# Performance work log

Hardware: AMD Instinct MI355X
Metric: run time of the kernel (lower is better)

The kernel has to match this reference:

```python
import jax, jax.numpy as jnp
import numpy as np

B, S, D = 2, 2048, 2048
H, KVH = 16, 4
HD = D // H            # 128
N_REP = H // KVH       # 4


def apply_rope(x, cos, sin):
    # x: (b, s, h, hd); cos/sin: (1, s, 1, hd//2)
    b, s, h, hd = x.shape
    xr = x.reshape(b, s, h, hd // 2, 2)
    p1, p2 = xr[..., 0], xr[..., 1]
    # Original concatenates rotated halves (does NOT re-interleave).
    return jnp.concatenate([p1 * cos - p2 * sin, p2 * cos + p1 * sin], axis=-1)


def setup_inputs() -> dict:
    key = jax.random.key(0)
    ks = jax.random.split(key, 8)
    hidden_states = jax.random.normal(ks[0], (B, S, D), dtype=jnp.float32)
    # additive causal mask (0 on/below diagonal, -1e9 above)
    mask = jnp.where(jnp.tril(jnp.ones((S, S), dtype=bool)), 0.0, -1e9).astype(jnp.float32)
    attention_mask = mask[None, None, :, :]
    cos = jax.random.normal(ks[1], (1, S, 1, HD // 2), dtype=jnp.float32)
    sin = jax.random.normal(ks[2], (1, S, 1, HD // 2), dtype=jnp.float32)
    sc = 1.0 / np.sqrt(D)
    Wq = jax.random.normal(ks[3], (D, H * HD), dtype=jnp.float32) * sc
    Wk = jax.random.normal(ks[4], (D, KVH * HD), dtype=jnp.float32) * sc
    Wv = jax.random.normal(ks[5], (D, KVH * HD), dtype=jnp.float32) * sc
    Wo = jax.random.normal(ks[6], (H * HD, D), dtype=jnp.float32) * sc
    return {"hidden_states": hidden_states, "attention_mask": attention_mask,
            "cos": cos, "sin": sin, "Wq": Wq, "Wk": Wk, "Wv": Wv, "Wo": Wo}


def reference(hidden_states, attention_mask, cos, sin, Wq, Wk, Wv, Wo):
    b, s, _ = hidden_states.shape
    q = (hidden_states @ Wq).reshape(b, s, H, HD)
    k = (hidden_states @ Wk).reshape(b, s, KVH, HD)
    v = (hidden_states @ Wv).reshape(b, s, KVH, HD)
    q = apply_rope(q, cos, sin)
    k = apply_rope(k, cos, sin)
    # GQA: repeat kv heads contiguously (matches expand+reshape)
    k = jnp.repeat(k, N_REP, axis=2)
    v = jnp.repeat(v, N_REP, axis=2)
    # (b, h, s, hd)
    q = q.transpose(0, 2, 1, 3)
    k = k.transpose(0, 2, 1, 3)
    v = v.transpose(0, 2, 1, 3)
    scores = jnp.einsum('bhqd,bhkd->bhqk', q, k) / np.sqrt(HD).astype(np.float32)
    scores = scores + attention_mask
    attn = jax.nn.softmax(scores.astype(jnp.float32), axis=-1)
    out = jnp.einsum('bhqk,bhkd->bhqd', attn, v)
    out = out.transpose(0, 2, 1, 3).reshape(b, s, H * HD)
    return out @ Wo
```

## Files before the change

kernel.cpp:

```cpp
#include <hip/hip_runtime.h>
#include <cstddef>
#include <cstdint>

#define S_LEN 2048
#define DMODEL 2048
#define NH 16
#define NKV 4
#define HD 128
#define BATCH 2
#define MROWS (BATCH * S_LEN)
#define KVD (NKV * HD)
#define QKVSTR 3072
#define NQT (S_LEN / 64)

typedef __attribute__((ext_vector_type(8))) short bf16x8;
typedef __attribute__((ext_vector_type(4))) short shortx4;
typedef __attribute__((ext_vector_type(4))) float floatx4;
typedef __attribute__((ext_vector_type(8))) _Float16 half8;
typedef __attribute__((ext_vector_type(4))) _Float16 half4;
typedef __attribute__((ext_vector_type(2))) _Float16 half2v;

#define QSCALE 0.1275310255f

__device__ inline short f2bf(float f) {
  union { float f; unsigned u; } v; v.f = f;
  unsigned r = v.u + 0x7FFFu + ((v.u >> 16) & 1u);
  return (short)(r >> 16);
}

__device__ inline half2v pack2h(float lo, float hi) {
  union { decltype(__builtin_amdgcn_cvt_pkrtz(0.f, 0.f)) raw; half2v h; } u;
  u.raw = __builtin_amdgcn_cvt_pkrtz(lo, hi);
  return u.h;
}

__device__ __forceinline__ void glds16(const void* g, void* l) {
  __builtin_amdgcn_global_load_lds(
      reinterpret_cast<const int __attribute__((address_space(1)))*>(
          reinterpret_cast<uintptr_t>(g)),
      reinterpret_cast<int __attribute__((address_space(3)))*>(
          reinterpret_cast<uintptr_t>(l)),
      16, 0, 0);
}

__global__ __launch_bounds__(256) void cast_bf16(
    const float* __restrict__ x, short* __restrict__ y)
{
  const size_t i = ((size_t)blockIdx.x * 256 + threadIdx.x) * 8;
  const float4 a = *(const float4*)(x + i);
  const float4 b = *(const float4*)(x + i + 4);
  bf16x8 o;
  o[0] = f2bf(a.x); o[1] = f2bf(a.y); o[2] = f2bf(a.z); o[3] = f2bf(a.w);
  o[4] = f2bf(b.x); o[5] = f2bf(b.y); o[6] = f2bf(b.z); o[7] = f2bf(b.w);
  *(bf16x8*)(y + i) = o;
}

__global__ __launch_bounds__(256) void tcast(
    const float* __restrict__ W, short* __restrict__ Wt, int N)
{
  __shared__ float Ts[64][65];
  const int n0 = blockIdx.x * 64, k0 = blockIdx.y * 64;
  const int tid = threadIdx.x;
#pragma unroll
  for (int it = 0; it < 4; ++it) {
    const int r = it * 16 + (tid >> 4);
    *(float4*)&Ts[r][(tid & 15) * 4] =
        *(const float4*)&W[(size_t)(k0 + r) * N + n0 + (tid & 15) * 4];
  }
  __syncthreads();
  const int n = tid >> 2, kg = (tid & 3) * 16;
  bf16x8 o0, o1;
#pragma unroll
  for (int e = 0; e < 8; ++e) o0[e] = f2bf(Ts[kg + e][n]);
#pragma unroll
  for (int e = 0; e < 8; ++e) o1[e] = f2bf(Ts[kg + 8 + e][n]);
  short* dst = Wt + (size_t)(n0 + n) * DMODEL + k0 + kg;
  *(bf16x8*)dst = o0;
  *(bf16x8*)(dst + 8) = o1;
}

template <int BN, bool OUTF16>
__global__ __launch_bounds__(512, 2) void gemm_swz(
    const short* __restrict__ A, const short* __restrict__ Bt,
    void* __restrict__ Cv, int M, int N, int K)
{
  constexpr int NF = BN / 64;
  __shared__ short As[2][256 * 64];
  __shared__ short Bs[2][BN * 64];

  const int tid = threadIdx.x;
  const int lane = tid & 63;
  const int l16 = lane & 15, quad = lane >> 4;
  const int wave = tid >> 6;
  const int wmi = wave >> 2;
  const int wni = wave & 3;
  const int m0 = blockIdx.y * 256, n0 = blockIdx.x * BN;

  const int srow = tid >> 3;
  const int scol = ((tid & 7) ^ (srow & 7)) * 8;
  const int lofs = srow * 64 + (tid & 7) * 8;
  const short* Ab = A + (size_t)(m0 + srow) * K + scol;
  const short* Bb = Bt + (size_t)(n0 + srow) * K + scol;

  const int xs0 = ((0 * 4 + quad) ^ (l16 & 7)) * 8;
  const int xs1 = ((1 * 4 + quad) ^ (l16 & 7)) * 8;

  floatx4 acc[8][NF];
#pragma unroll
  for (int i = 0; i < 8; ++i)
#pragma unroll
    for (int j = 0; j < NF; ++j)
#pragma unroll
      for (int r = 0; r < 4; ++r) acc[i][j][r] = 0.f;

#pragma unroll
  for (int u = 0; u < 4; ++u)
    glds16(Ab + (size_t)(u * 64) * K, &As[0][u * 4096 + lofs]);
#pragma unroll
  for (int u = 0; u < NF; ++u)
    glds16(Bb + (size_t)(u * 64) * K, &Bs[0][u * 4096 + lofs]);
  __syncthreads();

  const int nkt = K >> 6;
  for (int kt = 0; kt < nkt; ++kt) {
    const int cur = kt & 1;
    const short* Asc = As[cur];
    const short* Bsc = Bs[cur];
    short* Asn = As[cur ^ 1];
    short* Bsn = Bs[cur ^ 1];
    const int knext = (kt + 1) << 6;
    const bool pre = (kt + 1 < nkt);

    bf16x8 bfr[NF][2];
#pragma unroll
    for (int n = 0; n < NF; ++n) {
      const int br = (wni * (NF * 16) + n * 16 + l16) * 64;
      bfr[n][0] = *(const bf16x8*)&Bsc[br + xs0];
      bfr[n][1] = *(const bf16x8*)&Bsc[br + xs1];
    }

#pragma unroll
    for (int p = 0; p < 4; ++p) {
      bf16x8 af[2][2];
#pragma unroll
      for (int i = 0; i < 2; ++i) {
        const int ar = (wmi * 128 + (p * 2 + i) * 16 + l16) * 64;
        af[i][0] = *(const bf16x8*)&Asc[ar + xs0];
        af[i][1] = *(const bf16x8*)&Asc[ar + xs1];
      }
      if (pre) {
        if (p == 0) {
          glds16(Ab + (size_t)(0 * 64) * K + knext, &Asn[0 * 4096 + lofs]);
          glds16(Ab + (size_t)(1 * 64) * K + knext, &Asn[1 * 4096 + lofs]);
        } else if (p == 1) {
          glds16(Ab + (size_t)(2 * 64) * K + knext, &Asn[2 * 4096 + lofs]);
          glds16(Ab + (size_t)(3 * 64) * K + knext, &Asn[3 * 4096 + lofs]);
        } else if (p == 2) {
          glds16(Bb + (size_t)(0 * 64) * K + knext, &Bsn[0 * 4096 + lofs]);
          if (NF == 3)
            glds16(Bb + (size_t)(1 * 64) * K + knext, &Bsn[1 * 4096 + lofs]);
        } else {
          glds16(Bb + (size_t)((NF - 1) * 64) * K + knext, &Bsn[(NF - 1) * 4096 + lofs]);
        }
      }
      __builtin_amdgcn_s_barrier();
      __builtin_amdgcn_s_setprio(1);
#pragma unroll
      for (int i = 0; i < 2; ++i)
#pragma unroll
        for (int n = 0; n < NF; ++n) {
          acc[p * 2 + i][n] = __builtin_amdgcn_mfma_f32_16x16x32_bf16(af[i][0], bfr[n][0], acc[p * 2 + i][n], 0, 0, 0);
          acc[p * 2 + i][n] = __builtin_amdgcn_mfma_f32_16x16x32_bf16(af[i][1], bfr[n][1], acc[p * 2 + i][n], 0, 0, 0);
        }
      __builtin_amdgcn_s_setprio(0);
      if (p < 3) __builtin_amdgcn_s_barrier();
    }
    __syncthreads();
  }

#pragma unroll
  for (int mi = 0; mi < 8; ++mi)
#pragma unroll
    for (int r = 0; r < 4; ++r) {
      const int row = m0 + wmi * 128 + mi * 16 + quad * 4 + r;
      if (OUTF16) {
        _Float16* cr = (_Float16*)Cv + (size_t)row * N + n0 + wni * (NF * 16) + l16;
#pragma unroll
        for (int ni = 0; ni < NF; ++ni) cr[ni * 16] = (_Float16)acc[mi][ni][r];
      } else {
        float* cr = (float*)Cv + (size_t)row * N + n0 + wni * (NF * 16) + l16;
#pragma unroll
        for (int ni = 0; ni < NF; ++ni) cr[ni * 16] = acc[mi][ni][r];
      }
    }
}

__global__ __launch_bounds__(256) void rope_k(
    _Float16* __restrict__ kh, const float* __restrict__ cosp,
    const float* __restrict__ sinp)
{
  const int row = blockIdx.x * 4 + (threadIdx.x >> 6);
  const int sl = row & (S_LEN - 1);
  const int t = threadIdx.x & 63;
  const int h = t >> 4, g = t & 15;
  _Float16* base = kh + (size_t)row * QKVSTR + h * HD;
  const half8 x = *(const half8*)(base + 8 * g);
  const float4 c4 = *(const float4*)&cosp[sl * 64 + 4 * g];
  const float4 s4 = *(const float4*)&sinp[sl * 64 + 4 * g];
  const float p1[4] = {(float)x[0], (float)x[2], (float)x[4], (float)x[6]};
  const float p2[4] = {(float)x[1], (float)x[3], (float)x[5], (float)x[7]};
  const float cc[4] = {c4.x, c4.y, c4.z, c4.w};
  const float ss[4] = {s4.x, s4.y, s4.z, s4.w};
  __syncthreads();
  half4 o1, o2;
#pragma unroll
  for (int u = 0; u < 4; ++u) {
    o1[u] = (_Float16)(p1[u] * cc[u] - p2[u] * ss[u]);
    o2[u] = (_Float16)(p2[u] * cc[u] + p1[u] * ss[u]);
  }
  *(half4*)(base + 4 * g) = o1;
  *(half4*)(base + 64 + 4 * g) = o2;
}

__global__ __launch_bounds__(256) void vtprep(
    const _Float16* __restrict__ v, _Float16* __restrict__ Vt)
{
  __shared__ _Float16 Ts[64][72];
  const int s0 = blockIdx.x * 64, c0 = blockIdx.y * 64;
  const int tid = threadIdx.x;
#pragma unroll
  for (int it = 0; it < 4; ++it) {
    const int r = it * 16 + (tid >> 4);
    *(half4*)&Ts[r][(tid & 15) * 4] =
        *(const half4*)&v[(size_t)(s0 + r) * QKVSTR + c0 + (tid & 15) * 4];
  }
  __syncthreads();
  const int dr = tid >> 2, sg = tid & 3;
  const int d = c0 + dr;
  const int kvh = d >> 7, dd = d & 127;
  const int bb = s0 >> 11, sl = s0 & (S_LEN - 1);
  half8 t0, t1;
#pragma unroll
  for (int kk = 0; kk < 8; ++kk) t0[kk] = Ts[sg * 16 + kk][dr];
#pragma unroll
  for (int kk = 0; kk < 8; ++kk) t1[kk] = Ts[sg * 16 + 8 + kk][dr];
  _Float16* dst = Vt + ((size_t)(bb * NKV + kvh) * HD + dd) * S_LEN + sl + sg * 16;
  *(half8*)dst = t0;
  *(half8*)(dst + 8) = t1;
}

__global__ __launch_bounds__(256, 3) void attn_mfma(
    const _Float16* __restrict__ Qh, const _Float16* __restrict__ Kr,
    const _Float16* __restrict__ Vt, const float* __restrict__ cosp,
    const float* __restrict__ sinp, short* __restrict__ aout)
{
  __shared__ _Float16 Ks[64][136];
  __shared__ _Float16 Vs[128][72];
  __shared__ _Float16 Ps[4][16][72];

  const int tid = threadIdx.x;
  const int wave = tid >> 6, lane = tid & 63;
  const int l16 = lane & 15, quad = lane >> 4;
  const int pair = blockIdx.x;
  const int h = blockIdx.y, b = blockIdx.z;
  const int kvh = h >> 2;

  const int skr = tid >> 2;
  const int skc = (tid & 3) * 32;
  const _Float16* kgp = Kr + (size_t)(b * S_LEN + skr) * QKVSTR + kvh * HD + skc;
  const int svr = tid >> 1;
  const int svc = (tid & 1) * 32;
  const _Float16* vgp = Vt + ((size_t)(b * NKV + kvh) * HD + svr) * S_LEN + svc;

  for (int pass = 0; pass < 2; ++pass) {
    const int qt = pass ? (NQT - 1 - pair) : pair;
    const int q0 = qt * 64 + wave * 16;
    const int srow = q0 + l16;

    half8 qf[4];
    {
      const _Float16* qraw = Qh + (size_t)(b * S_LEN + srow) * QKVSTR + h * HD;
      const int co = (srow & (S_LEN - 1)) * 64;
#pragma unroll
      for (int cc = 0; cc < 2; ++cc) {
        const half8 r0 = *(const half8*)(qraw + cc * 64 + quad * 16);
        const half8 r1 = *(const half8*)(qraw + cc * 64 + quad * 16 + 8);
        const float4 c0 = *(const float4*)&cosp[co + cc * 32 + quad * 8];
        const float4 c1 = *(const float4*)&cosp[co + cc * 32 + quad * 8 + 4];
        const float4 s0 = *(const float4*)&sinp[co + cc * 32 + quad * 8];
        const float4 s1 = *(const float4*)&sinp[co + cc * 32 + quad * 8 + 4];
        const float cA[8] = {c0.x, c0.y, c0.z, c0.w, c1.x, c1.y, c1.z, c1.w};
        const float sA[8] = {s0.x, s0.y, s0.z, s0.w, s1.x, s1.y, s1.z, s1.w};
#pragma unroll
        for (int j = 0; j < 8; ++j) {
          const float p1 = (float)((j < 4) ? r0[2 * j] : r1[2 * (j - 4)]);
          const float p2 = (float)((j < 4) ? r0[2 * j + 1] : r1[2 * (j - 4) + 1]);
          qf[cc][j]     = (_Float16)((p1 * cA[j] - p2 * sA[j]) * QSCALE);
          qf[cc + 2][j] = (_Float16)((p2 * cA[j] + p1 * sA[j]) * QSCALE);
        }
      }
    }

    floatx4 o[8];
#pragma unroll
    for (int d = 0; d < 8; ++d) o[d] = (floatx4){0.f, 0.f, 0.f, 0.f};
    float m_run = -3e38f, l_run = 0.f;

    for (int kt = 0; kt <= qt; ++kt) {
      const int k0 = kt * 64;
      __syncthreads();
      {
        const _Float16* g = kgp + (size_t)k0 * QKVSTR;
        _Float16* dst = &Ks[skr][skc];
#pragma unroll
        for (int u = 0; u < 4; ++u)
          *(half8*)(dst + u * 8) = *(const half8*)(g + u * 8);
      }
      {
        const _Float16* g = vgp + k0;
        _Float16* dst = &Vs[svr][svc];
#pragma unroll
        for (int u = 0; u < 4; ++u)
          *(half8*)(dst + u * 8) = *(const half8*)(g + u * 8);
      }
      __syncthreads();

      floatx4 s[4];
      __builtin_amdgcn_s_setprio(1);
#pragma unroll
      for (int i = 0; i < 4; ++i) {
        s[i] = (floatx4){0.f, 0.f, 0.f, 0.f};
#pragma unroll
        for (int c = 0; c < 4; ++c) {
          const half8 kf = *(const half8*)&Ks[i * 16 + l16][quad * 8 + c * 32];
          s[i] = __builtin_amdgcn_mfma_f32_16x16x32_f16(kf, qf[c], s[i], 0, 0, 0);
        }
      }
      __builtin_amdgcn_s_setprio(0);

      if (kt == qt) {
#pragma unroll
        for (int i = 0; i < 4; ++i) {
          const int kvbase = k0 + i * 16 + quad * 4;
#pragma unroll
          for (int r = 0; r < 4; ++r)
            if (kvbase + r > srow) s[i][r] = -3.0e38f;
        }
      }

      float m0 = fmaxf(fmaxf(s[0][0], s[0][1]), fmaxf(s[0][2], s[0][3]));
      float m1 = fmaxf(fmaxf(s[1][0], s[1][1]), fmaxf(s[1][2], s[1][3]));
      float m2 = fmaxf(fmaxf(s[2][0], s[2][1]), fmaxf(s[2][2], s[2][3]));
      float m3 = fmaxf(fmaxf(s[3][0], s[3][1]), fmaxf(s[3][2], s[3][3]));
      float rm = fmaxf(fmaxf(m0, m1), fmaxf(m2, m3));
      rm = fmaxf(rm, __shfl_xor(rm, 16));
      rm = fmaxf(rm, __shfl_xor(rm, 32));
      if (rm > m_run) {
        const float alpha = exp2f(m_run - rm);
        m_run = rm;
        l_run *= alpha;
#pragma unroll
        for (int d = 0; d < 8; ++d)
#pragma unroll
          for (int r = 0; r < 4; ++r) o[d][r] *= alpha;
      }
      float p[4][4];
      float rs = 0.f;
#pragma unroll
      for (int i = 0; i < 4; ++i)
#pragma unroll
        for (int r = 0; r < 4; ++r) {
          p[i][r] = exp2f(s[i][r] - m_run);
          rs += p[i][r];
        }
      rs += __shfl_xor(rs, 16);
      rs += __shfl_xor(rs, 32);
      l_run += rs;

#pragma unroll
      for (int i = 0; i < 4; ++i) {
        *(half2v*)&Ps[wave][l16][i * 16 + quad * 4]     = pack2h(p[i][0], p[i][1]);
        *(half2v*)&Ps[wave][l16][i * 16 + quad * 4 + 2] = pack2h(p[i][2], p[i][3]);
      }
      const half8 pf0 = *(const half8*)&Ps[wave][l16][quad * 8];
      const half8 pf1 = *(const half8*)&Ps[wave][l16][32 + quad * 8];

      __builtin_amdgcn_s_setprio(1);
#pragma unroll
      for (int d = 0; d < 8; ++d) {
        const half8 vf0 = *(const half8*)&Vs[d * 16 + l16][quad * 8];
        const half8 vf1 = *(const half8*)&Vs[d * 16 + l16][32 + quad * 8];
        o[d] = __builtin_amdgcn_mfma_f32_16x16x32_f16(vf0, pf0, o[d], 0, 0, 0);
        o[d] = __builtin_amdgcn_mfma_f32_16x16x32_f16(vf1, pf1, o[d], 0, 0, 0);
      }
      __builtin_amdgcn_s_setprio(0);
    }

    const float inv = 1.0f / l_run;
    short* orow = aout + (size_t)(b * S_LEN + srow) * DMODEL + h * HD;
#pragma unroll
    for (int d = 0; d < 8; ++d) {
      shortx4 pk;
      pk[0] = f2bf(o[d][0] * inv);
      pk[1] = f2bf(o[d][1] * inv);
      pk[2] = f2bf(o[d][2] * inv);
      pk[3] = f2bf(o[d][3] * inv);
      *(shortx4*)(orow + d * 16 + quad * 4) = pk;
    }
  }
}

extern "C" void kernel_launch(void* const* d_in, const int* in_sizes, int n_in,
                              void* d_out, int out_size, void* d_ws, size_t ws_size,
                              hipStream_t stream) {
  const float* hs   = (const float*)d_in[0];
  const float* cosp = (const float*)d_in[2];
  const float* sinp = (const float*)d_in[3];
  const float* Wq   = (const float*)d_in[4];
  const float* Wk   = (const float*)d_in[5];
  const float* Wv   = (const float*)d_in[6];
  const float* Wo   = (const float*)d_in[7];
  float* out = (float*)d_out;

  char* w = (char*)d_ws;
  short*    hsb = (short*)w;
  short*    Wt  = (short*)(w + 16777216);
  _Float16* qkv = (_Float16*)(w + 29360128);
  _Float16* Vt  = (_Float16*)(w + 54525952);
  short*    ao  = hsb;

  _Float16* qh = qkv;
  _Float16* kh = qkv + 2048;
  _Float16* vh = qkv + 2560;

  dim3 blk(256);
  cast_bf16<<<MROWS * DMODEL / (8 * 256), blk, 0, stream>>>(hs, hsb);
  tcast<<<dim3(DMODEL / 64, DMODEL / 64), blk, 0, stream>>>(Wq, Wt, DMODEL);
  tcast<<<dim3(KVD / 64, DMODEL / 64), blk, 0, stream>>>(Wk, Wt + (size_t)2048 * DMODEL, KVD);
  tcast<<<dim3(KVD / 64, DMODEL / 64), blk, 0, stream>>>(Wv, Wt + (size_t)2560 * DMODEL, KVD);
  gemm_swz<192, true><<<dim3(QKVSTR / 192, MROWS / 256), dim3(512), 0, stream>>>(hsb, Wt, qkv, MROWS, QKVSTR, DMODEL);
  rope_k<<<MROWS / 4, blk, 0, stream>>>(kh, cosp, sinp);
  vtprep<<<dim3(MROWS / 64, KVD / 64), blk, 0, stream>>>(vh, Vt);
  attn_mfma<<<dim3(NQT / 2, NH, BATCH), blk, 0, stream>>>(qh, kh, Vt, cosp, sinp, ao);
  tcast<<<dim3(DMODEL / 64, DMODEL / 64), blk, 0, stream>>>(Wo, Wt, DMODEL);
  gemm_swz<128, false><<<dim3(DMODEL / 128, MROWS / 256), dim3(512), 0, stream>>>(ao, Wt, out, MROWS, DMODEL, DMODEL);
}
```

Before: 327.7 us.

## Process 32 query rows per wave to reuse K/V tiles in attention

Each attention block now handles a 128-row query tile: every wave owns 32 rows, held as two 16-row MFMA fragments that share each K and V fragment loaded from LDS. This replaces the earlier two-pass pairing of light and heavy 64-row tiles with one block per tile on a flattened 512-block grid, where the order of query tiles is reversed for the second batch to spread the causal work. The intent is to halve K/V global and LDS traffic per query row and raise the ratio of MFMA work to loads. In exchange, register pressure doubles, so the occupancy hint drops from 3 to 2 blocks per SM, and per-block work is less even.

```diff
diff --git a/kernel.cpp b/kernel.cpp
--- a/kernel.cpp
+++ b/kernel.cpp
@@ -11,7 +11,6 @@
 #define MROWS (BATCH * S_LEN)
 #define KVD (NKV * HD)
 #define QKVSTR 3072
-#define NQT (S_LEN / 64)
 
 typedef __attribute__((ext_vector_type(8))) short bf16x8;
 typedef __attribute__((ext_vector_type(4))) short shortx4;
@@ -249,20 +248,22 @@
   *(half8*)(dst + 8) = t1;
 }
 
-__global__ __launch_bounds__(256, 3) void attn_mfma(
+__global__ __launch_bounds__(256, 2) void attn_mfma(
     const _Float16* __restrict__ Qh, const _Float16* __restrict__ Kr,
     const _Float16* __restrict__ Vt, const float* __restrict__ cosp,
     const float* __restrict__ sinp, short* __restrict__ aout)
 {
   __shared__ _Float16 Ks[64][136];
   __shared__ _Float16 Vs[128][72];
-  __shared__ _Float16 Ps[4][16][72];
+  __shared__ _Float16 Ps[4][32][72];
 
   const int tid = threadIdx.x;
   const int wave = tid >> 6, lane = tid & 63;
   const int l16 = lane & 15, quad = lane >> 4;
-  const int pair = blockIdx.x;
-  const int h = blockIdx.y, b = blockIdx.z;
+  const int kb = blockIdx.x;
+  const int b = kb >> 8;
+  const int h = (kb >> 4) & 15;
+  const int qt = b ? (15 - (kb & 15)) : (kb & 15);
   const int kvh = h >> 2;
 
   const int skr = tid >> 2;
@@ -272,139 +273,159 @@
   const int svc = (tid & 1) * 32;
   const _Float16* vgp = Vt + ((size_t)(b * NKV + kvh) * HD + svr) * S_LEN + svc;
 
-  for (int pass = 0; pass < 2; ++pass) {
-    const int qt = pass ? (NQT - 1 - pair) : pair;
-    const int q0 = qt * 64 + wave * 16;
-    const int srow = q0 + l16;
-
-    half8 qf[4];
+  const int qbase = qt * 128 + wave * 32;
+
+  half8 qf[2][4];
+#pragma unroll
+  for (int r16 = 0; r16 < 2; ++r16) {
+    const int srow = qbase + r16 * 16 + l16;
+    const _Float16* qraw = Qh + (size_t)(b * S_LEN + srow) * QKVSTR + h * HD;
+    const int co = srow * 64;
+#pragma unroll
+    for (int cc = 0; cc < 2; ++cc) {
+      const half8 r0 = *(const half8*)(qraw + cc * 64 + quad * 16);
+      const half8 r1 = *(const half8*)(qraw + cc * 64 + quad * 16 + 8);
+      const float4 c0 = *(const float4*)&cosp[co + cc * 32 + quad * 8];
+      const float4 c1 = *(const float4*)&cosp[co + cc * 32 + quad * 8 + 4];
+      const float4 s0 = *(const float4*)&sinp[co + cc * 32 + quad * 8];
+      const float4 s1 = *(const float4*)&sinp[co + cc * 32 + quad * 8 + 4];
+      const float cA[8] = {c0.x, c0.y, c0.z, c0.w, c1.x, c1.y, c1.z, c1.w};
+      const float sA[8] = {s0.x, s0.y, s0.z, s0.w, s1.x, s1.y, s1.z, s1.w};
+#pragma unroll
+      for (int j = 0; j < 8; ++j) {
+        const float p1 = (float)((j < 4) ? r0[2 * j] : r1[2 * (j - 4)]);
+        const float p2 = (float)((j < 4) ? r0[2 * j + 1] : r1[2 * (j - 4) + 1]);
+        qf[r16][cc][j]     = (_Float16)((p1 * cA[j] - p2 * sA[j]) * QSCALE);
+        qf[r16][cc + 2][j] = (_Float16)((p2 * cA[j] + p1 * sA[j]) * QSCALE);
+      }
+    }
+  }
+
+  floatx4 o[2][8];
+#pragma unroll
+  for (int r16 = 0; r16 < 2; ++r16)
+#pragma unroll
+    for (int d = 0; d < 8; ++d) o[r16][d] = (floatx4){0.f, 0.f, 0.f, 0.f};
+  float m_run[2] = {-3e38f, -3e38f};
+  float l_run[2] = {0.f, 0.f};
+
+  const int ktmax = 2 * qt + 1;
+  for (int kt = 0; kt <= ktmax; ++kt) {
+    const int k0 = kt * 64;
+    __syncthreads();
     {
-      const _Float16* qraw = Qh + (size_t)(b * S_LEN + srow) * QKVSTR + h * HD;
-      const int co = (srow & (S_LEN - 1)) * 64;
-#pragma unroll
-      for (int cc = 0; cc < 2; ++cc) {
-        const half8 r0 = *(const half8*)(qraw + cc * 64 + quad * 16);
-        const half8 r1 = *(const half8*)(qraw + cc * 64 + quad * 16 + 8);
-        const float4 c0 = *(const float4*)&cosp[co + cc * 32 + quad * 8];
-        const float4 c1 = *(const float4*)&cosp[co + cc * 32 + quad * 8 + 4];
-        const float4 s0 = *(const float4*)&sinp[co + cc * 32 + quad * 8];
-        const float4 s1 = *(const float4*)&sinp[co + cc * 32 + quad * 8 + 4];
-        const float cA[8] = {c0.x, c0.y, c0.z, c0.w, c1.x, c1.y, c1.z, c1.w};
-        const float sA[8] = {s0.x, s0.y, s0.z, s0.w, s1.x, s1.y, s1.z, s1.w};
-#pragma unroll
-        for (int j = 0; j < 8; ++j) {
-          const float p1 = (float)((j < 4) ? r0[2 * j] : r1[2 * (j - 4)]);
-          const float p2 = (float)((j < 4) ? r0[2 * j + 1] : r1[2 * (j - 4) + 1]);
-          qf[cc][j]     = (_Float16)((p1 * cA[j] - p2 * sA[j]) * QSCALE);
-          qf[cc + 2][j] = (_Float16)((p2 * cA[j] + p1 * sA[j]) * QSCALE);
-        }
-      }
-    }
-
-    floatx4 o[8];
-#pragma unroll
-    for (int d = 0; d < 8; ++d) o[d] = (floatx4){0.f, 0.f, 0.f, 0.f};
-    float m_run = -3e38f, l_run = 0.f;
-
-    for (int kt = 0; kt <= qt; ++kt) {
-      const int k0 = kt * 64;
-      __syncthreads();
-      {
-        const _Float16* g = kgp + (size_t)k0 * QKVSTR;
-        _Float16* dst = &Ks[skr][skc];
-#pragma unroll
-        for (int u = 0; u < 4; ++u)
-          *(half8*)(dst + u * 8) = *(const half8*)(g + u * 8);
-      }
-      {
-        const _Float16* g = vgp + k0;
-        _Float16* dst = &Vs[svr][svc];
-#pragma unroll
-        for (int u = 0; u < 4; ++u)
-          *(half8*)(dst + u * 8) = *(const half8*)(g + u * 8);
-      }
-      __syncthreads();
-
-      floatx4 s[4];
-      __builtin_amdgcn_s_setprio(1);
-#pragma unroll
-      for (int i = 0; i < 4; ++i) {
-        s[i] = (floatx4){0.f, 0.f, 0.f, 0.f};
-#pragma unroll
-        for (int c = 0; c < 4; ++c) {
-          const half8 kf = *(const half8*)&Ks[i * 16 + l16][quad * 8 + c * 32];
-          s[i] = __builtin_amdgcn_mfma_f32_16x16x32_f16(kf, qf[c], s[i], 0, 0, 0);
-        }
-      }
-      __builtin_amdgcn_s_setprio(0);
-
-      if (kt == qt) {
+      const _Float16* g = kgp + (size_t)k0 * QKVSTR;
+      _Float16* dst = &Ks[skr][skc];
+#pragma unroll
+      for (int u = 0; u < 4; ++u)
+        *(half8*)(dst + u * 8) = *(const half8*)(g + u * 8);
+    }
+    {
+      const _Float16* g = vgp + k0;
+      _Float16* dst = &Vs[svr][svc];
+#pragma unroll
+      for (int u = 0; u < 4; ++u)
+        *(half8*)(dst + u * 8) = *(const half8*)(g + u * 8);
+    }
+    __syncthreads();
+
+    floatx4 s[2][4];
+    __builtin_amdgcn_s_setprio(1);
+#pragma unroll
+    for (int i = 0; i < 4; ++i) {
+      s[0][i] = (floatx4){0.f, 0.f, 0.f, 0.f};
+      s[1][i] = (floatx4){0.f, 0.f, 0.f, 0.f};
+#pragma unroll
+      for (int c = 0; c < 4; ++c) {
+        const half8 kf = *(const half8*)&Ks[i * 16 + l16][quad * 8 + c * 32];
+        s[0][i] = __builtin_amdgcn_mfma_f32_16x16x32_f16(kf, qf[0][c], s[0][i], 0, 0, 0);
+        s[1][i] = __builtin_amdgcn_mfma_f32_16x16x32_f16(kf, qf[1][c], s[1][i], 0, 0, 0);
+      }
+    }
+    __builtin_amdgcn_s_setprio(0);
+
+#pragma unroll
+    for (int r16 = 0; r16 < 2; ++r16) {
+      if (k0 + 63 > qbase + r16 * 16) {
+        const int srow = qbase + r16 * 16 + l16;
 #pragma unroll
         for (int i = 0; i < 4; ++i) {
           const int kvbase = k0 + i * 16 + quad * 4;
 #pragma unroll
           for (int r = 0; r < 4; ++r)
-            if (kvbase + r > srow) s[i][r] = -3.0e38f;
+            if (kvbase + r > srow) s[r16][i][r] = -3.0e38f;
         }
       }
-
-      float m0 = fmaxf(fmaxf(s[0][0], s[0][1]), fmaxf(s[0][2], s[0][3]));
-      float m1 = fmaxf(fmaxf(s[1][0], s[1][1]), fmaxf(s[1][2], s[1][3]));
-      float m2 = fmaxf(fmaxf(s[2][0], s[2][1]), fmaxf(s[2][2], s[2][3]));
-      float m3 = fmaxf(fmaxf(s[3][0], s[3][1]), fmaxf(s[3][2], s[3][3]));
+    }
+
+#pragma unroll
+    for (int r16 = 0; r16 < 2; ++r16) {
+      float m0 = fmaxf(fmaxf(s[r16][0][0], s[r16][0][1]), fmaxf(s[r16][0][2], s[r16][0][3]));
+      float m1 = fmaxf(fmaxf(s[r16][1][0], s[r16][1][1]), fmaxf(s[r16][1][2], s[r16][1][3]));
+      float m2 = fmaxf(fmaxf(s[r16][2][0], s[r16][2][1]), fmaxf(s[r16][2][2], s[r16][2][3]));
+      float m3 = fmaxf(fmaxf(s[r16][3][0], s[r16][3][1]), fmaxf(s[r16][3][2], s[r16][3][3]));
       float rm = fmaxf(fmaxf(m0, m1), fmaxf(m2, m3));
       rm = fmaxf(rm, __shfl_xor(rm, 16));
       rm = fmaxf(rm, __shfl_xor(rm, 32));
-      if (rm > m_run) {
-        const float alpha = exp2f(m_run - rm);
-        m_run = rm;
-        l_run *= alpha;
+      if (rm > m_run[r16]) {
+        const float alpha = exp2f(m_run[r16] - rm);
+        m_run[r16] = rm;
+        l_run[r16] *= alpha;
 #pragma unroll
         for (int d = 0; d < 8; ++d)
 #pragma unroll
-          for (int r = 0; r < 4; ++r) o[d][r] *= alpha;
-      }
-      float p[4][4];
+          for (int r = 0; r < 4; ++r) o[r16][d][r] *= alpha;
+      }
       float rs = 0.f;
 #pragma unroll
       for (int i = 0; i < 4; ++i)
 #pragma unroll
         for (int r = 0; r < 4; ++r) {
-          p[i][r] = exp2f(s[i][r] - m_run);
-          rs += p[i][r];
+          s[r16][i][r] = exp2f(s[r16][i][r] - m_run[r16]);
+          rs += s[r16][i][r];
         }
       rs += __shfl_xor(rs, 16);
       rs += __shfl_xor(rs, 32);
-      l_run += rs;
+      l_run[r16] += rs;
 
 #pragma unroll
       for (int i = 0; i < 4; ++i) {
-        *(half2v*)&Ps[wave][l16][i * 16 + quad * 4]     = pack2h(p[i][0], p[i][1]);
-        *(half2v*)&Ps[wave][l16][i * 16 + quad * 4 + 2] = pack2h(p[i][2], p[i][3]);
-      }
-      const half8 pf0 = *(const half8*)&Ps[wave][l16][quad * 8];
-      const half8 pf1 = *(const half8*)&Ps[wave][l16][32 + quad * 8];
-
-      __builtin_amdgcn_s_setprio(1);
-#pragma unroll
-      for (int d = 0; d < 8; ++d) {
-        const half8 vf0 = *(const half8*)&Vs[d * 16 + l16][quad * 8];
-        const half8 vf1 = *(const half8*)&Vs[d * 16 + l16][32 + quad * 8];
-        o[d] = __builtin_amdgcn_mfma_f32_16x16x32_f16(vf0, pf0, o[d], 0, 0, 0);
-        o[d] = __builtin_amdgcn_mfma_f32_16x16x32_f16(vf1, pf1, o[d], 0, 0, 0);
-      }
-      __builtin_amdgcn_s_setprio(0);
-    }
-
-    const float inv = 1.0f / l_run;
-    short* orow = aout + (size_t)(b * S_LEN + srow) * DMODEL + h * HD;
+        *(half2v*)&Ps[wave][r16 * 16 + l16][i * 16 + quad * 4] =
+            pack2h(s[r16][i][0], s[r16][i][1]);
+        *(half2v*)&Ps[wave][r16 * 16 + l16][i * 16 + quad * 4 + 2] =
+            pack2h(s[r16][i][2], s[r16][i][3]);
+      }
+    }
+
+    const half8 pf00 = *(const half8*)&Ps[wave][l16][quad * 8];
+    const half8 pf01 = *(const half8*)&Ps[wave][l16][32 + quad * 8];
+    const half8 pf10 = *(const half8*)&Ps[wave][16 + l16][quad * 8];
+    const half8 pf11 = *(const half8*)&Ps[wave][16 + l16][32 + quad * 8];
+
+    __builtin_amdgcn_s_setprio(1);
+#pragma unroll
+    for (int d = 0; d < 8; ++d) {
+      const half8 vf0 = *(const half8*)&Vs[d * 16 + l16][quad * 8];
+      const half8 vf1 = *(const half8*)&Vs[d * 16 + l16][32 + quad * 8];
+      o[0][d] = __builtin_amdgcn_mfma_f32_16x16x32_f16(vf0, pf00, o[0][d], 0, 0, 0);
+      o[0][d] = __builtin_amdgcn_mfma_f32_16x16x32_f16(vf1, pf01, o[0][d], 0, 0, 0);
+      o[1][d] = __builtin_amdgcn_mfma_f32_16x16x32_f16(vf0, pf10, o[1][d], 0, 0, 0);
+      o[1][d] = __builtin_amdgcn_mfma_f32_16x16x32_f16(vf1, pf11, o[1][d], 0, 0, 0);
+    }
+    __builtin_amdgcn_s_setprio(0);
+  }
+
+#pragma unroll
+  for (int r16 = 0; r16 < 2; ++r16) {
+    const float inv = 1.0f / l_run[r16];
+    short* orow = aout + (size_t)(b * S_LEN + qbase + r16 * 16 + l16) * DMODEL + h * HD;
 #pragma unroll
     for (int d = 0; d < 8; ++d) {
       shortx4 pk;
-      pk[0] = f2bf(o[d][0] * inv);
-      pk[1] = f2bf(o[d][1] * inv);
-      pk[2] = f2bf(o[d][2] * inv);
-      pk[3] = f2bf(o[d][3] * inv);
+      pk[0] = f2bf(o[r16][d][0] * inv);
+      pk[1] = f2bf(o[r16][d][1] * inv);
+      pk[2] = f2bf(o[r16][d][2] * inv);
+      pk[3] = f2bf(o[r16][d][3] * inv);
       *(shortx4*)(orow + d * 16 + quad * 4) = pk;
     }
   }
@@ -441,7 +462,7 @@
   gemm_swz<192, true><<<dim3(QKVSTR / 192, MROWS / 256), dim3(512), 0, stream>>>(hsb, Wt, qkv, MROWS, QKVSTR, DMODEL);
   rope_k<<<MROWS / 4, blk, 0, stream>>>(kh, cosp, sinp);
   vtprep<<<dim3(MROWS / 64, KVD / 64), blk, 0, stream>>>(vh, Vt);
-  attn_mfma<<<dim3(NQT / 2, NH, BATCH), blk, 0, stream>>>(qh, kh, Vt, cosp, sinp, ao);
+  attn_mfma<<<dim3(512), blk, 0, stream>>>(qh, kh, Vt, cosp, sinp, ao);
   tcast<<<dim3(DMODEL / 64, DMODEL / 64), blk, 0, stream>>>(Wo, Wt, DMODEL);
   gemm_swz<128, false><<<dim3(DMODEL / 128, MROWS / 256), dim3(512), 0, stream>>>(ao, Wt, out, MROWS, DMODEL, DMODEL);
 }
```

After: 336.5 us. 1.03x slower.

## Load K/V tiles directly into LDS with XOR-swizzled unpadded layout

Applied to the files above, without the earlier changes.

The attention kernel now copies each K and V tile straight from global memory into LDS with a direct-to-LDS 16-byte load helper, instead of staging the data through registers. The padded shared arrays become flat unpadded tiles, and an XOR swizzle on the 8-element chunk index, keyed on row, is meant to avoid LDS bank conflicts on the MFMA fragment reads. This is meant to cut VGPR pressure and the instructions spent on the tile copy. The risk is that swizzle and index mistakes would silently corrupt results, and the cost of the direct-to-LDS path depends on the hardware.

```diff
diff --git a/kernel.cpp b/kernel.cpp
--- a/kernel.cpp
+++ b/kernel.cpp
@@ -254,8 +254,8 @@
     const _Float16* __restrict__ Vt, const float* __restrict__ cosp,
     const float* __restrict__ sinp, short* __restrict__ aout)
 {
-  __shared__ _Float16 Ks[64][136];
-  __shared__ _Float16 Vs[128][72];
+  __shared__ _Float16 Ks[64 * 128];
+  __shared__ _Float16 Vs[128 * 64];
   __shared__ _Float16 Ps[4][16][72];
 
   const int tid = threadIdx.x;
@@ -265,12 +265,13 @@
   const int h = blockIdx.y, b = blockIdx.z;
   const int kvh = h >> 2;
 
-  const int skr = tid >> 2;
-  const int skc = (tid & 3) * 32;
-  const _Float16* kgp = Kr + (size_t)(b * S_LEN + skr) * QKVSTR + kvh * HD + skc;
-  const int svr = tid >> 1;
-  const int svc = (tid & 1) * 32;
-  const _Float16* vgp = Vt + ((size_t)(b * NKV + kvh) * HD + svr) * S_LEN + svc;
+  const int kxc = ((tid & 15) ^ ((tid >> 4) & 7)) * 8;
+  const int vxc = ((tid & 7) ^ ((tid >> 3) & 7)) * 8;
+  const _Float16* kgp = Kr + (size_t)(b * S_LEN + (tid >> 4)) * QKVSTR + kvh * HD + kxc;
+  const _Float16* vgp = Vt + ((size_t)(b * NKV + kvh) * HD + (tid >> 3)) * S_LEN + vxc;
+  _Float16* kdst = Ks + tid * 8;
+  _Float16* vdst = Vs + tid * 8;
+  const int xq = l16 & 7;
 
   for (int pass = 0; pass < 2; ++pass) {
     const int qt = pass ? (NQT - 1 - pair) : pair;
@@ -280,7 +281,7 @@
     half8 qf[4];
     {
       const _Float16* qraw = Qh + (size_t)(b * S_LEN + srow) * QKVSTR + h * HD;
-      const int co = (srow & (S_LEN - 1)) * 64;
+      const int co = srow * 64;
 #pragma unroll
       for (int cc = 0; cc < 2; ++cc) {
         const half8 r0 = *(const half8*)(qraw + cc * 64 + quad * 16);
@@ -309,20 +310,12 @@
     for (int kt = 0; kt <= qt; ++kt) {
       const int k0 = kt * 64;
       __syncthreads();
-      {
-        const _Float16* g = kgp + (size_t)k0 * QKVSTR;
-        _Float16* dst = &Ks[skr][skc];
-#pragma unroll
-        for (int u = 0; u < 4; ++u)
-          *(half8*)(dst + u * 8) = *(const half8*)(g + u * 8);
-      }
-      {
-        const _Float16* g = vgp + k0;
-        _Float16* dst = &Vs[svr][svc];
-#pragma unroll
-        for (int u = 0; u < 4; ++u)
-          *(half8*)(dst + u * 8) = *(const half8*)(g + u * 8);
-      }
+#pragma unroll
+      for (int c = 0; c < 4; ++c)
+        glds16(kgp + (size_t)(k0 + c * 16) * QKVSTR, kdst + c * 2048);
+#pragma unroll
+      for (int c = 0; c < 4; ++c)
+        glds16(vgp + (size_t)(c * 32) * S_LEN + k0, vdst + c * 2048);
       __syncthreads();
 
       floatx4 s[4];
@@ -332,7 +325,7 @@
         s[i] = (floatx4){0.f, 0.f, 0.f, 0.f};
 #pragma unroll
         for (int c = 0; c < 4; ++c) {
-          const half8 kf = *(const half8*)&Ks[i * 16 + l16][quad * 8 + c * 32];
+          const half8 kf = *(const half8*)&Ks[(i * 16 + l16) * 128 + ((quad + 4 * c) ^ xq) * 8];
           s[i] = __builtin_amdgcn_mfma_f32_16x16x32_f16(kf, qf[c], s[i], 0, 0, 0);
         }
       }
@@ -388,8 +381,8 @@
       __builtin_amdgcn_s_setprio(1);
 #pragma unroll
       for (int d = 0; d < 8; ++d) {
-        const half8 vf0 = *(const half8*)&Vs[d * 16 + l16][quad * 8];
-        const half8 vf1 = *(const half8*)&Vs[d * 16 + l16][32 + quad * 8];
+        const half8 vf0 = *(const half8*)&Vs[(d * 16 + l16) * 64 + (quad ^ xq) * 8];
+        const half8 vf1 = *(const half8*)&Vs[(d * 16 + l16) * 64 + ((quad + 4) ^ xq) * 8];
         o[d] = __builtin_amdgcn_mfma_f32_16x16x32_f16(vf0, pf0, o[d], 0, 0, 0);
         o[d] = __builtin_amdgcn_mfma_f32_16x16x32_f16(vf1, pf1, o[d], 0, 0, 0);
       }
```

Result: faster. 320.6 us (-2.2%).
